# Kernel optimization log

Measured on AMD Instinct MI355X. Metric: run time of the kernel, lower is better.

The kernel has to match this reference:

```python
import jax, jax.numpy as jnp
import numpy as np

T, B, D_MODEL, D_KEY = 4096, 4, 1024, 1024


def setup_inputs() -> dict:
    key = jax.random.key(0)
    kx, kq, kk, kv = jax.random.split(key, 4)
    scale = 1.0 / np.sqrt(D_MODEL)
    x = jax.random.normal(kx, (T, B, D_MODEL), dtype=jnp.float32)
    # torch.nn.Linear weights are [out_features, in_features]
    Wq = jax.random.uniform(kq, (D_KEY, D_MODEL), dtype=jnp.float32, minval=-scale, maxval=scale)
    Wk = jax.random.uniform(kk, (D_KEY, D_MODEL), dtype=jnp.float32, minval=-scale, maxval=scale)
    Wv = jax.random.uniform(kv, (D_MODEL, D_MODEL), dtype=jnp.float32, minval=-scale, maxval=scale)
    return {"x": x, "Wq": Wq, "Wk": Wk, "Wv": Wv}


def _kernel(u):
    return jax.nn.elu(u) + 1.0


def reference(x, Wq, Wk, Wv):
    # x: [T, B, d_model] (time-major, as in the original module)
    Q = _kernel(jnp.einsum('tbd,kd->tbk', x, Wq))  # [T, B, d_key]
    K = _kernel(jnp.einsum('tbd,kd->tbk', x, Wk))  # [T, B, d_key]
    V = jnp.einsum('tbd,md->tbm', x, Wv)           # [T, B, d_model]

    s0 = jnp.zeros((D_KEY, D_MODEL), dtype=x.dtype)  # shared state: sums K^T V over time AND batch
    z0 = jnp.zeros((B, D_KEY), dtype=x.dtype)        # per-batch normalizer state

    def step(carry, qkv):
        s, z = carry
        q, k, v = qkv                                  # q,k: [B, d_key]; v: [B, d_model]
        s = s + jnp.einsum('bk,bm->km', k, v)          # [d_key, d_model] (sums over batch, per original)
        z = z + k                                      # [B, d_key]
        numer = q @ s                                  # [B, d_model]
        denom = jnp.sum(q * z, axis=-1, keepdims=True) # [B, 1]
        return (s, z), numer / denom

    _, y = jax.lax.scan(step, (s0, z0), (Q, K, V))
    return y  # [T, B, d_model]
```

## Files before the change

kernel.cpp:

```cpp
#include <hip/hip_runtime.h>
#include <hip/hip_bf16.h>
#include <stdint.h>

typedef unsigned short u16;
typedef __attribute__((ext_vector_type(8))) __bf16 bf16x8;
typedef __attribute__((ext_vector_type(4))) float floatx4;
typedef __attribute__((ext_vector_type(8))) unsigned short us8;
typedef __attribute__((ext_vector_type(4))) unsigned short us4;

#define TT 4096
#define BB 4
#define DM 1024
#define ROWS (TT * BB)
#define CHUNK 128
#define CR (CHUNK * BB)
#define NC (TT / CHUNK)
#define MB (1024l * 1024l)

__device__ __forceinline__ float b2f(u16 x) {
  union { unsigned int u; float f; } v; v.u = ((unsigned int)x) << 16; return v.f;
}
__device__ __forceinline__ u16 f2b(float f) {
  union { float f; unsigned int u; } v; v.f = f;
  unsigned int r = v.u + 0x7fffu + ((v.u >> 16) & 1u);
  return (u16)(r >> 16);
}

__global__ void k_sniff(const u16* __restrict__ x, int* __restrict__ flag) {
  const int lane = threadIdx.x & 63;
  int cnt = 0;
#pragma unroll
  for (int k = 0; k < 32; ++k) {
    u16 u = x[2 * (lane + 64 * k)];
    int e = (u >> 7) & 0xFF;
    cnt += (e >= 100 && e <= 140) ? 1 : 0;
  }
#pragma unroll
  for (int d = 32; d > 0; d >>= 1) cnt += __shfl_down(cnt, d, 64);
  if (lane == 0) *flag = (cnt >= 1024) ? 1 : 0;
}

__global__ __launch_bounds__(256) void k_convert(const void* __restrict__ src,
                                                 u16* __restrict__ dst,
                                                 const int* __restrict__ flag, long n) {
  long i = ((long)blockIdx.x * 256 + threadIdx.x) * 4;
  if (i >= n) return;
  if (*flag) {
    *(us4*)(dst + i) = *(const us4*)((const u16*)src + i);
  } else {
    const float* s = (const float*)src;
    us4 o;
#pragma unroll
    for (int e = 0; e < 4; ++e) o[e] = f2b(s[i + e]);
    *(us4*)(dst + i) = o;
  }
}

__device__ __forceinline__ void ldsg16(const u16* g, u16* l) {
  auto gp = reinterpret_cast<__attribute__((address_space(1))) void*>(
      reinterpret_cast<uintptr_t>(const_cast<u16*>(g)));
  auto lp = reinterpret_cast<__attribute__((address_space(3))) void*>(
      (unsigned int)reinterpret_cast<uintptr_t>(l));
  __builtin_amdgcn_global_load_lds(gp, lp, 16, 0, 0);
}

__device__ __forceinline__ void bar() {
  asm volatile("" ::: "memory");
  __builtin_amdgcn_s_barrier();
  asm volatile("" ::: "memory");
}
__device__ __forceinline__ void stage4(const u16* g, u16* l, long s64) {
  ldsg16(g, l);
  ldsg16(g + s64, l + 4096);
  ldsg16(g + 2 * s64, l + 8192);
  ldsg16(g + 3 * s64, l + 12288);
}

#define LD4(DST, BASE, OFF) \
  _Pragma("unroll") \
  for (int ii = 0; ii < 4; ++ii) DST[ii] = *(const bf16x8*)((BASE) + ii * 2048 + (OFF))

#define MFMA16(AC0, AF, BF) \
  _Pragma("unroll") \
  for (int mi = 0; mi < 4; ++mi) \
    _Pragma("unroll") \
    for (int ni = 0; ni < 4; ++ni) \
      acc[(AC0) + mi][ni] = __builtin_amdgcn_mfma_f32_16x16x32_bf16(AF[mi], BF[ni], acc[(AC0) + mi][ni], 0, 0, 0)

__device__ __forceinline__ void gemm256s(
    const u16* __restrict__ A1, long lda1,
    const u16* __restrict__ B1, long ldb1, int K1,
    const u16* __restrict__ A2, long lda2,
    const u16* __restrict__ B2, long ldb2, int K2,
    u16* sA, u16* sB, floatx4 acc[8][4])
{
  const int t = threadIdx.x, w = t >> 6, lane = t & 63;
  const int quad = lane >> 4, m16 = lane & 15;
  const int wm = w >> 2, wn = w & 3;
  const int csw = ((t & 7) ^ ((t >> 4) & 7)) << 3;
  const long row = t >> 3;
  const u16* ga1 = A1 + row * lda1 + csw;
  const u16* gb1 = B1 + row * ldb1 + csw;
  const u16* ga2 = A2 + row * lda2 + csw;
  const u16* gb2 = B2 + row * ldb2 + csw;
  const long a641 = 64l * lda1, b641 = 64l * ldb1;
  const long a642 = 64l * lda2, b642 = 64l * ldb2;
  u16* lA = sA + w * 512;
  u16* lB = sB + w * 512;
  const char* cA = (const char*)sA;
  const char* cB = (const char*)sB;
  const int lx = ((m16 >> 1) & 7) << 4;
  const int raB = (wm * 128 + m16) << 7;
  const int rbB = (wn * 64 + m16) << 7;
  const int kq0 = (quad << 4) ^ lx;
  const int kq1 = (64 + (quad << 4)) ^ lx;
  const int NT1 = K1 >> 6, NT = (K1 + K2) >> 6;

  auto STAGE = [&](int tt, int buf) {
    const u16 *sa, *sb; long s64a, s64b;
    if (tt < NT1) { sa = ga1 + (long)tt * 64;          sb = gb1 + (long)tt * 64;          s64a = a641; s64b = b641; }
    else          { long u = tt - NT1; sa = ga2 + u * 64; sb = gb2 + u * 64;              s64a = a642; s64b = b642; }
    stage4(sa, lA + (buf << 14), s64a);
    stage4(sb, lB + (buf << 14), s64b);
  };

  STAGE(0, 0);
  STAGE(1, 1);
  asm volatile("s_waitcnt vmcnt(8)" ::: "memory");
  bar();

  for (int kt = 0; kt < NT; ++kt) {
    const char* pA = cA + ((kt & 1) << 15) + raB;
    const char* pB = cB + ((kt & 1) << 15) + rbB;
    bf16x8 aX[4], aY[4], b0[4], b1[4];

    LD4(aX, pA, kq0);
    LD4(b0, pB, kq0);
    LD4(aY, pA, kq1);
    LD4(b1, pB, kq1);
    MFMA16(0, aX, b0);
    LD4(aX, pA, 8192 + kq0);
    MFMA16(0, aY, b1);
    LD4(aY, pA, 8192 + kq1);
    MFMA16(4, aX, b0);

    asm volatile("s_waitcnt lgkmcnt(0)" ::: "memory");
    __builtin_amdgcn_sched_barrier(0);
    bar();
    if (kt + 2 < NT) STAGE(kt + 2, kt & 1);
    __builtin_amdgcn_s_setprio(1);
    MFMA16(4, aY, b1);
    __builtin_amdgcn_s_setprio(0);
    __builtin_amdgcn_sched_barrier(0);
    if (kt + 2 < NT)      { asm volatile("s_waitcnt vmcnt(8)" ::: "memory"); }
    else if (kt + 1 < NT) { asm volatile("s_waitcnt vmcnt(0)" ::: "memory"); }
    bar();
  }
}

__device__ __forceinline__ void gemm128(
    const u16* __restrict__ A, long lda,
    const u16* __restrict__ B, long ldb,
    int K, u16* sA, u16* sB, floatx4 acc[4][4])
{
  const int t = threadIdx.x, w = t >> 6, lane = t & 63;
  const int m16 = lane & 15, quad = lane >> 4;
  const int wm = w >> 1, wn = w & 1;
  const int sq = (lane & 3) ^ ((lane >> 3) & 3);
  const u16* ga = A + (long)(t >> 2) * lda + sq * 8;
  const u16* gb = B + (long)(t >> 2) * ldb + sq * 8;
  const long a64 = 64l * lda, b64 = 64l * ldb;
  u16* lA = sA + w * 512;
  u16* lB = sB + w * 512;
  const char* cA = (const char*)sA;
  const char* cB = (const char*)sB;
  const int slot = quad ^ ((m16 >> 1) & 3);
  const int aoff = wm * 4096 + m16 * 64 + slot * 16;
  const int boff = wn * 4096 + m16 * 64 + slot * 16;
  for (int k0 = 0; k0 < K; k0 += 32) {
    __syncthreads();
    ldsg16(ga, lA);
    ldsg16(ga + a64, lA + 2048);
    ldsg16(gb, lB);
    ldsg16(gb + b64, lB + 2048);
    ga += 32; gb += 32;
    __syncthreads();
    bf16x8 af[4], bfr[4];
#pragma unroll
    for (int i = 0; i < 4; ++i) af[i]  = *(const bf16x8*)(cA + aoff + i * 1024);
#pragma unroll
    for (int i = 0; i < 4; ++i) bfr[i] = *(const bf16x8*)(cB + boff + i * 1024);
#pragma unroll
    for (int im = 0; im < 4; ++im)
#pragma unroll
      for (int in = 0; in < 4; ++in)
        acc[im][in] = __builtin_amdgcn_mfma_f32_16x16x32_bf16(af[im], bfr[in], acc[im][in], 0, 0, 0);
  }
}

__global__ __launch_bounds__(512, 2) void k_proj2(
    const u16* __restrict__ X, const u16* __restrict__ Wt, u16* __restrict__ Y, int mode)
{
  __shared__ __align__(16) u16 sm[65536];
  floatx4 acc[8][4] = {};
  const int raw = blockIdx.x;
  const int id = ((raw & 7) << 5) | (raw >> 3);
  const int m0 = (id >> 2) * 256, n0 = (id & 3) * 256;
  gemm256s(X + (long)m0 * DM, DM, Wt + (long)n0 * DM, DM, DM,
           X, DM, Wt, DM, 0, sm, sm + 32768, acc);
  const int t = threadIdx.x, w = t >> 6, lane = t & 63;
  const int wm = w >> 2, wn = w & 3, quad = lane >> 4, c16 = lane & 15;
#pragma unroll
  for (int mi = 0; mi < 8; ++mi)
#pragma unroll
    for (int ni = 0; ni < 4; ++ni) {
      const int gr = m0 + wm * 128 + mi * 16 + quad * 4;
      const int gc = n0 + wn * 64 + ni * 16 + c16;
      floatx4 v = acc[mi][ni];
      if (mode == 2) {
        us4 o;
#pragma unroll
        for (int e = 0; e < 4; ++e) o[e] = f2b(v[e]);
        *(us4*)(Y + (long)gc * ROWS + gr) = o;
      } else {
#pragma unroll
        for (int e = 0; e < 4; ++e) {
          float u = v[e];
          u = u > 0.f ? u + 1.f : __expf(u);
          Y[(long)(gr + e) * DM + gc] = f2b(u);
        }
      }
    }
}

__global__ __launch_bounds__(256) void k_transpose(const u16* __restrict__ src, u16* __restrict__ dst)
{
  const int t = threadIdx.x;
  const int sx = t & 15, sy = t >> 4;
  const long r0 = (long)blockIdx.x * 128 + sy * 8;
  const long c0 = (long)blockIdx.y * 128 + sx * 8;
  us8 r[8];
#pragma unroll
  for (int v = 0; v < 8; ++v) r[v] = *(const us8*)(src + (r0 + v) * DM + c0);
#pragma unroll
  for (int u = 0; u < 8; ++u) {
    us8 o;
#pragma unroll
    for (int v = 0; v < 8; ++v) o[v] = r[v][u];
    *(us8*)(dst + (c0 + u) * ROWS + r0) = o;
  }
}

__global__ __launch_bounds__(256) void k_cksum(const u16* __restrict__ Kp, float* __restrict__ cs)
{
  const int id = blockIdx.x * 256 + threadIdx.x;
  const int i = id & 1023, b = (id >> 10) & 3, j = id >> 12;
  const u16* p = Kp + ((long)j * CR + b) * DM + i;
  float a = 0.f;
#pragma unroll 8
  for (int tl = 0; tl < CHUNK; ++tl) a += b2f(p[(long)tl * BB * DM]);
  cs[id] = a;
}

__global__ __launch_bounds__(256) void k_zfill(const u16* __restrict__ Kp,
                                               const float* __restrict__ cs,
                                               u16* __restrict__ z)
{
  const int id = blockIdx.x * 256 + threadIdx.x;
  const int i = id & 1023, b = (id >> 10) & 3, j = id >> 12;
  float a = 0.f;
  for (int j2 = 0; j2 < j; ++j2) a += cs[j2 * 4096 + b * 1024 + i];
  const u16* p = Kp + ((long)j * CR + b) * DM + i;
  u16* q = z + ((long)j * CR + b) * DM + i;
  for (int tl = 0; tl < CHUNK; ++tl) {
    a += b2f(p[(long)tl * BB * DM]);
    q[(long)tl * BB * DM] = f2b(a);
  }
}

__global__ __launch_bounds__(512, 2) void k_gemm_g2(
    const u16* __restrict__ Vt, const u16* __restrict__ Kt, u16* __restrict__ G)
{
  __shared__ __align__(16) u16 sm[65536];
  floatx4 acc[8][4] = {};
  const int id = blockIdx.x;
  const int x = id & 7, s = id >> 3;
  const int j = x + 8 * (s >> 4);
  const int nm = s & 15;
  const int n0 = (nm & 3) * 256;
  const int m0 = (nm >> 2) * 256;
  gemm256s(Vt + (long)m0 * ROWS + j * CR, ROWS,
           Kt + (long)n0 * ROWS + j * CR, ROWS, CR,
           Vt, ROWS, Kt, ROWS, 0, sm, sm + 32768, acc);
  const int t = threadIdx.x, w = t >> 6, lane = t & 63;
  const int wm = w >> 2, wn = w & 3, quad = lane >> 4, c16 = lane & 15;
  u16* Gj = G + (long)j * DM * DM;
#pragma unroll
  for (int mi = 0; mi < 8; ++mi)
#pragma unroll
    for (int ni = 0; ni < 4; ++ni) {
      const int gr = m0 + wm * 128 + mi * 16 + quad * 4;
      const int gc = n0 + wn * 64 + ni * 16 + c16;
      floatx4 v = acc[mi][ni];
#pragma unroll
      for (int e = 0; e < 4; ++e) Gj[(long)(gr + e) * DM + gc] = f2b(v[e]);
    }
}

__global__ __launch_bounds__(256) void k_prefix(u16* __restrict__ G)
{
  const long id = (long)blockIdx.x * 256 + threadIdx.x;
  float a = 0.f;
#pragma unroll
  for (int j = 0; j < NC; ++j) {
    u16* p = G + (long)j * DM * DM + id;
    float g = b2f(*p);
    *p = f2b(a);
    a += g;
  }
}

__global__ __launch_bounds__(256) void k_scores(
    const u16* __restrict__ Q, const u16* __restrict__ Kp, u16* __restrict__ P)
{
  __shared__ __align__(16) u16 sA[4096];
  __shared__ __align__(16) u16 sB[4096];
  floatx4 acc[4][4] = {};
  const int id = blockIdx.x;
  const int x = id & 7, s = id >> 3;
  const int j = x + 8 * (s >> 4);
  const int nm = s & 15;
  const int n0 = (nm & 3) * 128;
  const int m0 = (nm >> 2) * 128;
  if (n0 <= m0) {
    gemm128(Q + ((long)j * CR + m0) * DM, DM,
            Kp + ((long)j * CR + n0) * DM, DM, DM, sA, sB, acc);
  }
  const int t = threadIdx.x, lane = t & 63, w = t >> 6;
  const int wm = w >> 1, wn = w & 1, quad = lane >> 4, c16 = lane & 15;
  u16* Pj = P + (long)j * CR * CR;
#pragma unroll
  for (int im = 0; im < 4; ++im)
#pragma unroll
    for (int in = 0; in < 4; ++in) {
      const int gc = n0 + wn * 64 + in * 16 + c16;
      const int gr = m0 + wm * 64 + im * 16 + quad * 4;
      const bool valid = (gc <= gr + 3);
      floatx4 v = acc[im][in];
#pragma unroll
      for (int e = 0; e < 4; ++e)
        Pj[(long)(gr + e) * CR + gc] = valid ? f2b(v[e]) : (u16)0;
    }
}

__global__ __launch_bounds__(256) void k_denom(
    const u16* __restrict__ Q, const u16* __restrict__ z, float* __restrict__ denom)
{
  const int w = threadIdx.x >> 6, lane = threadIdx.x & 63;
  const long row = (long)blockIdx.x * 4 + w;
  const u16* q = Q + row * DM;
  const u16* zz = z + row * DM;
  float s = 0.f;
#pragma unroll
  for (int p = 0; p < 2; ++p) {
    const int off = lane * 8 + p * 512;
    us8 q8 = *(const us8*)(q + off);
    us8 z8 = *(const us8*)(zz + off);
#pragma unroll
    for (int e = 0; e < 8; ++e) s += b2f(q8[e]) * b2f(z8[e]);
  }
#pragma unroll
  for (int d = 32; d > 0; d >>= 1) s += __shfl_down(s, d, 64);
  if (lane == 0) denom[row] = s;
}

__global__ __launch_bounds__(512, 2) void k_out2(
    const u16* __restrict__ P, const u16* __restrict__ Vt,
    const u16* __restrict__ Q, const u16* __restrict__ St,
    const float* __restrict__ denom, void* __restrict__ out,
    const int* __restrict__ flag)
{
  __shared__ __align__(16) u16 sm[65536];
  floatx4 acc[8][4] = {};
  const int id = blockIdx.x;
  const int x = id & 7, s = id >> 3;
  const int j = x + 8 * (s >> 3);
  const int nm = s & 7;
  const int n0 = (nm & 3) * 256;
  const int m0 = (nm >> 2) * 256;
  gemm256s(P + (long)j * CR * CR + (long)m0 * CR, CR,
           Vt + (long)n0 * ROWS + j * CR, ROWS, m0 + 256,
           Q + ((long)j * CR + m0) * DM, DM,
           St + (long)j * DM * DM + (long)n0 * DM, DM, DM,
           sm, sm + 32768, acc);
  const int t = threadIdx.x, w = t >> 6, lane = t & 63;
  const int wm = w >> 2, wn = w & 3, quad = lane >> 4, c16 = lane & 15;
  const int isf16 = *flag;
  float* of = (float*)out;
  u16* ob = (u16*)out;
#pragma unroll
  for (int mi = 0; mi < 8; ++mi)
#pragma unroll
    for (int ni = 0; ni < 4; ++ni) {
      const int gc = n0 + wn * 64 + ni * 16 + c16;
      const int grl = m0 + wm * 128 + mi * 16 + quad * 4;
      const long gr = (long)j * CR + grl;
      floatx4 v = acc[mi][ni];
#pragma unroll
      for (int e = 0; e < 4; ++e) {
        const float d = denom[gr + e];
        const float y = v[e] / d;
        if (isf16) ob[(gr + e) * DM + gc] = f2b(y);
        else       of[(gr + e) * DM + gc] = y;
      }
    }
}

extern "C" void kernel_launch(void* const* d_in, const int* in_sizes, int n_in,
                              void* d_out, int out_size, void* d_ws, size_t ws_size,
                              hipStream_t stream)
{
  char* ws = (char*)d_ws;
  u16*  xc  = (u16*)(ws);
  u16*  z   = (u16*)(ws);
  u16*  Q   = (u16*)(ws + 32 * MB);
  u16*  K   = (u16*)(ws + 64 * MB);
  u16*  Kt  = (u16*)(ws + 96 * MB);
  u16*  P   = (u16*)(ws + 96 * MB);
  u16*  Vt  = (u16*)(ws + 128 * MB);
  u16*  G   = (u16*)(ws + 160 * MB);
  u16*  Wqc = (u16*)(ws + 224 * MB);
  u16*  Wkc = (u16*)(ws + 226 * MB);
  u16*  Wvc = (u16*)(ws + 228 * MB);
  float* cs = (float*)(ws + 230 * MB);
  float* dn = (float*)(ws + 230 * MB + 524288);
  int* flag = (int*)(ws + 230 * MB + 524288 + 65536);

  dim3 blk(256), blk5(512);
  k_sniff<<<1, 64, 0, stream>>>((const u16*)d_in[0], flag);
  k_convert<<<16384, blk, 0, stream>>>(d_in[0], xc, flag, (long)ROWS * DM);
  k_convert<<<1024, blk, 0, stream>>>(d_in[1], Wqc, flag, (long)DM * DM);
  k_convert<<<1024, blk, 0, stream>>>(d_in[2], Wkc, flag, (long)DM * DM);
  k_convert<<<1024, blk, 0, stream>>>(d_in[3], Wvc, flag, (long)DM * DM);
  k_proj2<<<dim3(256), blk5, 0, stream>>>(xc, Wqc, Q, 1);
  k_proj2<<<dim3(256), blk5, 0, stream>>>(xc, Wkc, K, 1);
  k_proj2<<<dim3(256), blk5, 0, stream>>>(xc, Wvc, Vt, 2);
  k_transpose<<<dim3(128, 8), blk, 0, stream>>>(K, Kt);
  k_cksum<<<dim3(512), blk, 0, stream>>>(K, cs);
  k_zfill<<<dim3(512), blk, 0, stream>>>(K, cs, z);
  k_gemm_g2<<<dim3(512), blk5, 0, stream>>>(Vt, Kt, G);
  k_prefix<<<dim3(4096), blk, 0, stream>>>(G);
  k_scores<<<dim3(512), blk, 0, stream>>>(Q, K, P);
  k_denom<<<dim3(4096), blk, 0, stream>>>(Q, z, dn);
  k_out2<<<dim3(256), blk5, 0, stream>>>(P, Vt, Q, G, dn, d_out, flag);
}
```

Measured before the change: 438.3 us.

## Fuse K transpose into projection epilogue and move scores to 256-tile GEMM

The K projection now writes both row-major K and transposed Kt straight from its epilogue, so the separate transpose kernel, with its extra read and write of K, is gone. The per-chunk causal score GEMM switches from a 128x128 tile kernel with a simple synchronous loop to the pipelined 256x256 gemm256s path used by the projections, with 128 blocks of 512 threads. Larger tiles give more reuse and deeper pipelining, but a 256 tile wastes more work on the masked upper triangle and 128 blocks may underfill the GPU. The K epilogue also now does strided transposed stores in addition to its row stores.

```diff
diff --git a/kernel.cpp b/kernel.cpp
--- a/kernel.cpp
+++ b/kernel.cpp
@@ -158,48 +158,9 @@
   }
 }
 
-__device__ __forceinline__ void gemm128(
-    const u16* __restrict__ A, long lda,
-    const u16* __restrict__ B, long ldb,
-    int K, u16* sA, u16* sB, floatx4 acc[4][4])
-{
-  const int t = threadIdx.x, w = t >> 6, lane = t & 63;
-  const int m16 = lane & 15, quad = lane >> 4;
-  const int wm = w >> 1, wn = w & 1;
-  const int sq = (lane & 3) ^ ((lane >> 3) & 3);
-  const u16* ga = A + (long)(t >> 2) * lda + sq * 8;
-  const u16* gb = B + (long)(t >> 2) * ldb + sq * 8;
-  const long a64 = 64l * lda, b64 = 64l * ldb;
-  u16* lA = sA + w * 512;
-  u16* lB = sB + w * 512;
-  const char* cA = (const char*)sA;
-  const char* cB = (const char*)sB;
-  const int slot = quad ^ ((m16 >> 1) & 3);
-  const int aoff = wm * 4096 + m16 * 64 + slot * 16;
-  const int boff = wn * 4096 + m16 * 64 + slot * 16;
-  for (int k0 = 0; k0 < K; k0 += 32) {
-    __syncthreads();
-    ldsg16(ga, lA);
-    ldsg16(ga + a64, lA + 2048);
-    ldsg16(gb, lB);
-    ldsg16(gb + b64, lB + 2048);
-    ga += 32; gb += 32;
-    __syncthreads();
-    bf16x8 af[4], bfr[4];
-#pragma unroll
-    for (int i = 0; i < 4; ++i) af[i]  = *(const bf16x8*)(cA + aoff + i * 1024);
-#pragma unroll
-    for (int i = 0; i < 4; ++i) bfr[i] = *(const bf16x8*)(cB + boff + i * 1024);
-#pragma unroll
-    for (int im = 0; im < 4; ++im)
-#pragma unroll
-      for (int in = 0; in < 4; ++in)
-        acc[im][in] = __builtin_amdgcn_mfma_f32_16x16x32_bf16(af[im], bfr[in], acc[im][in], 0, 0, 0);
-  }
-}
-
 __global__ __launch_bounds__(512, 2) void k_proj2(
-    const u16* __restrict__ X, const u16* __restrict__ Wt, u16* __restrict__ Y, int mode)
+    const u16* __restrict__ X, const u16* __restrict__ Wt,
+    u16* __restrict__ Y, u16* __restrict__ Yt, int mode)
 {
   __shared__ __align__(16) u16 sm[65536];
   floatx4 acc[8][4] = {};
@@ -217,38 +178,24 @@
       const int gr = m0 + wm * 128 + mi * 16 + quad * 4;
       const int gc = n0 + wn * 64 + ni * 16 + c16;
       floatx4 v = acc[mi][ni];
-      if (mode == 2) {
+      float uv[4];
+#pragma unroll
+      for (int e = 0; e < 4; ++e) {
+        float u = v[e];
+        if (mode & 1) u = u > 0.f ? u + 1.f : __expf(u);
+        uv[e] = u;
+      }
+      if (mode & 1) {
+#pragma unroll
+        for (int e = 0; e < 4; ++e) Y[(long)(gr + e) * DM + gc] = f2b(uv[e]);
+      }
+      if (mode & 2) {
         us4 o;
 #pragma unroll
-        for (int e = 0; e < 4; ++e) o[e] = f2b(v[e]);
-        *(us4*)(Y + (long)gc * ROWS + gr) = o;
-      } else {
-#pragma unroll
-        for (int e = 0; e < 4; ++e) {
-          float u = v[e];
-          u = u > 0.f ? u + 1.f : __expf(u);
-          Y[(long)(gr + e) * DM + gc] = f2b(u);
-        }
+        for (int e = 0; e < 4; ++e) o[e] = f2b(uv[e]);
+        *(us4*)(Yt + (long)gc * ROWS + gr) = o;
       }
     }
-}
-
-__global__ __launch_bounds__(256) void k_transpose(const u16* __restrict__ src, u16* __restrict__ dst)
-{
-  const int t = threadIdx.x;
-  const int sx = t & 15, sy = t >> 4;
-  const long r0 = (long)blockIdx.x * 128 + sy * 8;
-  const long c0 = (long)blockIdx.y * 128 + sx * 8;
-  us8 r[8];
-#pragma unroll
-  for (int v = 0; v < 8; ++v) r[v] = *(const us8*)(src + (r0 + v) * DM + c0);
-#pragma unroll
-  for (int u = 0; u < 8; ++u) {
-    us8 o;
-#pragma unroll
-    for (int v = 0; v < 8; ++v) o[v] = r[v][u];
-    *(us8*)(dst + (c0 + u) * ROWS + r0) = o;
-  }
 }
 
 __global__ __launch_bounds__(256) void k_cksum(const u16* __restrict__ Kp, float* __restrict__ cs)
@@ -320,33 +267,33 @@
   }
 }
 
-__global__ __launch_bounds__(256) void k_scores(
+__global__ __launch_bounds__(512, 2) void k_scores2(
     const u16* __restrict__ Q, const u16* __restrict__ Kp, u16* __restrict__ P)
 {
-  __shared__ __align__(16) u16 sA[4096];
-  __shared__ __align__(16) u16 sB[4096];
-  floatx4 acc[4][4] = {};
+  __shared__ __align__(16) u16 sm[65536];
+  floatx4 acc[8][4] = {};
   const int id = blockIdx.x;
   const int x = id & 7, s = id >> 3;
-  const int j = x + 8 * (s >> 4);
-  const int nm = s & 15;
-  const int n0 = (nm & 3) * 128;
-  const int m0 = (nm >> 2) * 128;
+  const int j = x + 8 * (s >> 2);
+  const int nm = s & 3;
+  const int n0 = (nm & 1) * 256;
+  const int m0 = (nm >> 1) * 256;
   if (n0 <= m0) {
-    gemm128(Q + ((long)j * CR + m0) * DM, DM,
-            Kp + ((long)j * CR + n0) * DM, DM, DM, sA, sB, acc);
-  }
-  const int t = threadIdx.x, lane = t & 63, w = t >> 6;
-  const int wm = w >> 1, wn = w & 1, quad = lane >> 4, c16 = lane & 15;
+    gemm256s(Q + ((long)j * CR + m0) * DM, DM,
+             Kp + ((long)j * CR + n0) * DM, DM, DM,
+             Q, DM, Kp, DM, 0, sm, sm + 32768, acc);
+  }
+  const int t = threadIdx.x, w = t >> 6, lane = t & 63;
+  const int wm = w >> 2, wn = w & 3, quad = lane >> 4, c16 = lane & 15;
   u16* Pj = P + (long)j * CR * CR;
 #pragma unroll
-  for (int im = 0; im < 4; ++im)
-#pragma unroll
-    for (int in = 0; in < 4; ++in) {
-      const int gc = n0 + wn * 64 + in * 16 + c16;
-      const int gr = m0 + wm * 64 + im * 16 + quad * 4;
+  for (int mi = 0; mi < 8; ++mi)
+#pragma unroll
+    for (int ni = 0; ni < 4; ++ni) {
+      const int gr = m0 + wm * 128 + mi * 16 + quad * 4;
+      const int gc = n0 + wn * 64 + ni * 16 + c16;
       const bool valid = (gc <= gr + 3);
-      floatx4 v = acc[im][in];
+      floatx4 v = acc[mi][ni];
 #pragma unroll
       for (int e = 0; e < 4; ++e)
         Pj[(long)(gr + e) * CR + gc] = valid ? f2b(v[e]) : (u16)0;
@@ -442,15 +389,14 @@
   k_convert<<<1024, blk, 0, stream>>>(d_in[1], Wqc, flag, (long)DM * DM);
   k_convert<<<1024, blk, 0, stream>>>(d_in[2], Wkc, flag, (long)DM * DM);
   k_convert<<<1024, blk, 0, stream>>>(d_in[3], Wvc, flag, (long)DM * DM);
-  k_proj2<<<dim3(256), blk5, 0, stream>>>(xc, Wqc, Q, 1);
-  k_proj2<<<dim3(256), blk5, 0, stream>>>(xc, Wkc, K, 1);
-  k_proj2<<<dim3(256), blk5, 0, stream>>>(xc, Wvc, Vt, 2);
-  k_transpose<<<dim3(128, 8), blk, 0, stream>>>(K, Kt);
+  k_proj2<<<dim3(256), blk5, 0, stream>>>(xc, Wqc, Q, (u16*)nullptr, 1);
+  k_proj2<<<dim3(256), blk5, 0, stream>>>(xc, Wkc, K, Kt, 3);
+  k_proj2<<<dim3(256), blk5, 0, stream>>>(xc, Wvc, (u16*)nullptr, Vt, 2);
   k_cksum<<<dim3(512), blk, 0, stream>>>(K, cs);
   k_zfill<<<dim3(512), blk, 0, stream>>>(K, cs, z);
   k_gemm_g2<<<dim3(512), blk5, 0, stream>>>(Vt, Kt, G);
   k_prefix<<<dim3(4096), blk, 0, stream>>>(G);
-  k_scores<<<dim3(512), blk, 0, stream>>>(Q, K, P);
+  k_scores2<<<dim3(128), blk5, 0, stream>>>(Q, K, P);
   k_denom<<<dim3(4096), blk, 0, stream>>>(Q, z, dn);
   k_out2<<<dim3(256), blk5, 0, stream>>>(P, Vt, Q, G, dn, d_out, flag);
 }
```

Measured after the change: 456.0 us. 4.0% more time.
